# Kernel optimization log

Hardware: AMD Instinct MI355X
Metric: run time of the kernel (lower is better)

Reference implementation:

```python
import jax, jax.numpy as jnp
import numpy as np

SIG_T_TRAIN = 0.07
SIG_T_INFER = 0.07
EPS = 1e-12  # torch F.normalize eps


def _l2_normalize(x):
    # matches torch.nn.functional.normalize(x, dim=-1): x / max(||x||_2, eps)
    nrm = jnp.sqrt(jnp.sum(x * x, axis=-1, keepdims=True))
    return x / jnp.maximum(nrm, EPS)


def setup_inputs() -> dict:
    key = jax.random.key(0)
    k1, k2 = jax.random.split(key)
    v_feat = jax.random.normal(k1, (32, 16, 256, 512), dtype=jnp.float32)  # (b,n,t,d)
    t_feat = jax.random.normal(k2, (512, 512), dtype=jnp.float32)          # (c,d)
    return {"v_feat": v_feat, "t_feat": t_feat, "split": 1}


def reference(v_feat, t_feat, split):
    # split: 1 -> 'test' (normalize + sig_T_infer), 0 -> train (sig_T_train)
    if split == 1:
        tau = SIG_T_INFER
        v_feat = _l2_normalize(v_feat)
        t_feat = _l2_normalize(t_feat)
    else:
        tau = SIG_T_TRAIN
    # Original: dist = einsum('bntd,bmcd->bctnm', v, t_repeated)/tau, then mean over m, then n.
    # t_repeated is identical along m (a pure repeat), so mean over m is a no-op, and the
    # mean over n commutes with the linear contraction: reduce over n first, never
    # materializing the (b,c,t,n,m) tensor.
    v_mean = jnp.mean(v_feat, axis=1)  # (b,t,d)
    dist = jnp.einsum('btd,cd->bct', v_mean, t_feat) / tau  # (b,c,t)
    return dist
```

## Files before the change

### kernel.cpp

```cpp
#include <hip/hip_runtime.h>

typedef unsigned short u16;
typedef unsigned int u32;

typedef __bf16 bf16x8 __attribute__((ext_vector_type(8)));
typedef float f32x4 __attribute__((ext_vector_type(4)));

__device__ __forceinline__ u16 f2bf(float f) {
    u32 u = __float_as_uint(f);
    return (u16)((u + 0x7fffu + ((u >> 16) & 1u)) >> 16);
}

__device__ __forceinline__ float rowreduce64(float s) {
#pragma unroll
    for (int off = 32; off > 0; off >>= 1) s += __shfl_xor(s, off, 64);
    return s;
}

constexpr int LDK = 520;

__global__ __launch_bounds__(512, 2) void fused_kernel(
    const float* __restrict__ v,
    const float* __restrict__ tf,
    float* __restrict__ out,
    const int* __restrict__ splitp)
{
    const int b    = blockIdx.y;
    const int t0   = blockIdx.x * 32;
    const int tid  = threadIdx.x;
    const int w    = tid >> 6;
    const int lane = tid & 63;
    const int quad = lane >> 4;
    const int l15  = lane & 15;
    const int split = *splitp;

    __shared__ u16 At[64 * LDK];
    __shared__ u16 Bt[32 * LDK];

    for (int tt = 0; tt < 4; tt++) {
        const int tl = w * 4 + tt;
        float acc[8];
#pragma unroll
        for (int i = 0; i < 8; i++) acc[i] = 0.f;
#pragma unroll 4
        for (int n = 0; n < 16; n++) {
            const float* row = v + (((size_t)(b * 16 + n) * 256 + (t0 + tl)) * 512) + lane * 8;
            float4 x0 = *reinterpret_cast<const float4*>(row);
            float4 x1 = *reinterpret_cast<const float4*>(row + 4);
            float s = x0.x*x0.x + x0.y*x0.y + x0.z*x0.z + x0.w*x0.w
                    + x1.x*x1.x + x1.y*x1.y + x1.z*x1.z + x1.w*x1.w;
            s = rowreduce64(s);
            float inv = 1.0f;
            if (split == 1) inv = 1.0f / fmaxf(sqrtf(s), 1e-12f);
            acc[0] += x0.x*inv; acc[1] += x0.y*inv;
            acc[2] += x0.z*inv; acc[3] += x0.w*inv;
            acc[4] += x1.x*inv; acc[5] += x1.y*inv;
            acc[6] += x1.z*inv; acc[7] += x1.w*inv;
        }
        uint4 pk;
        pk.x = (u32)f2bf(acc[0]*0.0625f) | ((u32)f2bf(acc[1]*0.0625f) << 16);
        pk.y = (u32)f2bf(acc[2]*0.0625f) | ((u32)f2bf(acc[3]*0.0625f) << 16);
        pk.z = (u32)f2bf(acc[4]*0.0625f) | ((u32)f2bf(acc[5]*0.0625f) << 16);
        pk.w = (u32)f2bf(acc[6]*0.0625f) | ((u32)f2bf(acc[7]*0.0625f) << 16);
        *reinterpret_cast<uint4*>(&Bt[tl * LDK + lane * 8]) = pk;
    }

    const int wm = w & 3;
    const int wn = w >> 2;
    const float sc = 1.0f / 0.07f;
    float* ob = out + (size_t)b * 131072;

    for (int cc = 0; cc < 8; cc++) {
#pragma unroll
        for (int rr = 0; rr < 8; rr++) {
            const int r = w * 8 + rr;
            const float* rp = tf + (size_t)(cc * 64 + r) * 512 + lane * 8;
            float4 x0 = *reinterpret_cast<const float4*>(rp);
            float4 x1 = *reinterpret_cast<const float4*>(rp + 4);
            float s = x0.x*x0.x + x0.y*x0.y + x0.z*x0.z + x0.w*x0.w
                    + x1.x*x1.x + x1.y*x1.y + x1.z*x1.z + x1.w*x1.w;
            s = rowreduce64(s);
            float inv = 1.0f;
            if (split == 1) inv = 1.0f / fmaxf(sqrtf(s), 1e-12f);
            uint4 pk;
            pk.x = (u32)f2bf(x0.x*inv) | ((u32)f2bf(x0.y*inv) << 16);
            pk.y = (u32)f2bf(x0.z*inv) | ((u32)f2bf(x0.w*inv) << 16);
            pk.z = (u32)f2bf(x1.x*inv) | ((u32)f2bf(x1.y*inv) << 16);
            pk.w = (u32)f2bf(x1.z*inv) | ((u32)f2bf(x1.w*inv) << 16);
            *reinterpret_cast<uint4*>(&At[r * LDK + lane * 8]) = pk;
        }
        __syncthreads();

        f32x4 acc = {0.f, 0.f, 0.f, 0.f};
#pragma unroll
        for (int kk = 0; kk < 512; kk += 32) {
            bf16x8 af = *reinterpret_cast<const bf16x8*>(
                &At[(wm * 16 + l15) * LDK + kk + quad * 8]);
            bf16x8 bf = *reinterpret_cast<const bf16x8*>(
                &Bt[(wn * 16 + l15) * LDK + kk + quad * 8]);
            acc = __builtin_amdgcn_mfma_f32_16x16x32_bf16(af, bf, acc, 0, 0, 0);
        }
        __syncthreads();

#pragma unroll
        for (int r = 0; r < 4; r++) {
            const int c = cc * 64 + wm * 16 + quad * 4 + r;
            ob[c * 256 + (t0 + wn * 16 + l15)] = acc[r] * sc;
        }
    }
}

extern "C" void kernel_launch(void* const* d_in, const int* in_sizes, int n_in,
                              void* d_out, int out_size, void* d_ws, size_t ws_size,
                              hipStream_t stream) {
    const float* v_feat = (const float*)d_in[0];
    const float* t_feat = (const float*)d_in[1];
    const int*   splitp = (const int*)d_in[2];
    float* out = (float*)d_out;

    (void)d_ws; (void)ws_size;

    fused_kernel<<<dim3(8, 32), dim3(512), 0, stream>>>(v_feat, t_feat, out, splitp);
}
```

Before: 426.6 us.

## Split fused kernel into parallel prep pass and separate MFMA GEMM kernel

```diff
diff --git a/kernel.cpp b/kernel.cpp
--- a/kernel.cpp
+++ b/kernel.cpp
@@ -11,103 +11,148 @@
     return (u16)((u + 0x7fffu + ((u >> 16) & 1u)) >> 16);
 }
 
-__device__ __forceinline__ float rowreduce64(float s) {
-#pragma unroll
-    for (int off = 32; off > 0; off >>= 1) s += __shfl_xor(s, off, 64);
-    return s;
-}
-
-constexpr int LDK = 520;
-
-__global__ __launch_bounds__(512, 2) void fused_kernel(
+__global__ __launch_bounds__(256, 4) void prep_kernel(
     const float* __restrict__ v,
     const float* __restrict__ tf,
-    float* __restrict__ out,
+    u16* __restrict__ vm,
+    u16* __restrict__ tn,
     const int* __restrict__ splitp)
 {
-    const int b    = blockIdx.y;
-    const int t0   = blockIdx.x * 32;
     const int tid  = threadIdx.x;
     const int w    = tid >> 6;
     const int lane = tid & 63;
+    const int g    = lane >> 4;
+    const int l15  = lane & 15;
+    const int split = *splitp;
+    const int bxx  = blockIdx.x;
+
+    if (bxx >= 8192) {
+        const int row = (bxx - 8192) * 16 + w * 4 + g;
+        const float* rp = tf + (size_t)row * 512;
+        float4 x[8];
+#pragma unroll
+        for (int i = 0; i < 8; i++)
+            x[i] = *reinterpret_cast<const float4*>(rp + i * 64 + l15 * 4);
+        float s = 0.f;
+#pragma unroll
+        for (int i = 0; i < 8; i++)
+            s += x[i].x*x[i].x + x[i].y*x[i].y + x[i].z*x[i].z + x[i].w*x[i].w;
+#pragma unroll
+        for (int off = 1; off < 16; off <<= 1) s += __shfl_xor(s, off, 64);
+        float inv = 1.0f;
+        if (split == 1) inv = 1.0f / fmaxf(sqrtf(s), 1e-12f);
+        u16* orow = tn + (size_t)row * 512;
+#pragma unroll
+        for (int i = 0; i < 8; i++) {
+            uint2 pk;
+            pk.x = (u32)f2bf(x[i].x*inv) | ((u32)f2bf(x[i].y*inv) << 16);
+            pk.y = (u32)f2bf(x[i].z*inv) | ((u32)f2bf(x[i].w*inv) << 16);
+            *reinterpret_cast<uint2*>(orow + i * 64 + l15 * 4) = pk;
+        }
+        return;
+    }
+
+    const int b = bxx >> 8;
+    const int t = bxx & 255;
+    const int n = w * 4 + g;
+    const float* rp = v + (((size_t)(b * 16 + n) * 256) + t) * 512;
+
+    float4 x[8];
+#pragma unroll
+    for (int i = 0; i < 8; i++)
+        x[i] = *reinterpret_cast<const float4*>(rp + i * 64 + l15 * 4);
+
+    float s = 0.f;
+#pragma unroll
+    for (int i = 0; i < 8; i++)
+        s += x[i].x*x[i].x + x[i].y*x[i].y + x[i].z*x[i].z + x[i].w*x[i].w;
+#pragma unroll
+    for (int off = 1; off < 16; off <<= 1) s += __shfl_xor(s, off, 64);
+    float inv = 1.0f;
+    if (split == 1) inv = 1.0f / fmaxf(sqrtf(s), 1e-12f);
+
+#pragma unroll
+    for (int i = 0; i < 8; i++) {
+        x[i].x *= inv; x[i].y *= inv; x[i].z *= inv; x[i].w *= inv;
+    }
+
+#pragma unroll
+    for (int off = 16; off < 64; off <<= 1)
+#pragma unroll
+        for (int i = 0; i < 8; i++) {
+            x[i].x += __shfl_xor(x[i].x, off, 64);
+            x[i].y += __shfl_xor(x[i].y, off, 64);
+            x[i].z += __shfl_xor(x[i].z, off, 64);
+            x[i].w += __shfl_xor(x[i].w, off, 64);
+        }
+
+    __shared__ float lds[4][512];
+#pragma unroll
+    for (int j = 0; j < 2; j++) {
+        const int i = 2 * g + j;
+        *reinterpret_cast<float4*>(&lds[w][i * 64 + l15 * 4]) = x[i];
+    }
+    __syncthreads();
+
+    float2 r; r.x = 0.f; r.y = 0.f;
+#pragma unroll
+    for (int w2 = 0; w2 < 4; w2++) {
+        float2 p = *reinterpret_cast<const float2*>(&lds[w2][tid * 2]);
+        r.x += p.x; r.y += p.y;
+    }
+    r.x *= 0.0625f; r.y *= 0.0625f;
+    u32 packed = (u32)f2bf(r.x) | ((u32)f2bf(r.y) << 16);
+    reinterpret_cast<u32*>(vm)[((size_t)(b * 256 + t) << 8) + tid] = packed;
+}
+
+__global__ __launch_bounds__(256) void gemm_kernel(
+    const u16* __restrict__ tn,
+    const u16* __restrict__ vm,
+    float* __restrict__ out)
+{
+    const int tid  = threadIdx.x;
+    const int lane = tid & 63;
+    const int wid  = tid >> 6;
+    const int wm   = wid & 1;
+    const int wn   = wid >> 1;
     const int quad = lane >> 4;
     const int l15  = lane & 15;
-    const int split = *splitp;
 
-    __shared__ u16 At[64 * LDK];
-    __shared__ u16 Bt[32 * LDK];
+    const int c0 = blockIdx.x * 64 + wm * 32;
+    const int t0 = blockIdx.y * 64 + wn * 32;
+    const int b  = blockIdx.z;
 
-    for (int tt = 0; tt < 4; tt++) {
-        const int tl = w * 4 + tt;
-        float acc[8];
+    const u16* A0 = tn + (size_t)(c0 + l15) * 512 + quad * 8;
+    const u16* B0 = vm + (size_t)b * 131072 + (size_t)(t0 + l15) * 512 + quad * 8;
+
+    f32x4 acc[2][2] = {};
+#pragma unroll 4
+    for (int kk = 0; kk < 512; kk += 32) {
+        bf16x8 af[2], bf[2];
 #pragma unroll
-        for (int i = 0; i < 8; i++) acc[i] = 0.f;
-#pragma unroll 4
-        for (int n = 0; n < 16; n++) {
-            const float* row = v + (((size_t)(b * 16 + n) * 256 + (t0 + tl)) * 512) + lane * 8;
-            float4 x0 = *reinterpret_cast<const float4*>(row);
-            float4 x1 = *reinterpret_cast<const float4*>(row + 4);
-            float s = x0.x*x0.x + x0.y*x0.y + x0.z*x0.z + x0.w*x0.w
-                    + x1.x*x1.x + x1.y*x1.y + x1.z*x1.z + x1.w*x1.w;
-            s = rowreduce64(s);
-            float inv = 1.0f;
-            if (split == 1) inv = 1.0f / fmaxf(sqrtf(s), 1e-12f);
-            acc[0] += x0.x*inv; acc[1] += x0.y*inv;
-            acc[2] += x0.z*inv; acc[3] += x0.w*inv;
-            acc[4] += x1.x*inv; acc[5] += x1.y*inv;
-            acc[6] += x1.z*inv; acc[7] += x1.w*inv;
-        }
-        uint4 pk;
-        pk.x = (u32)f2bf(acc[0]*0.0625f) | ((u32)f2bf(acc[1]*0.0625f) << 16);
-        pk.y = (u32)f2bf(acc[2]*0.0625f) | ((u32)f2bf(acc[3]*0.0625f) << 16);
-        pk.z = (u32)f2bf(acc[4]*0.0625f) | ((u32)f2bf(acc[5]*0.0625f) << 16);
-        pk.w = (u32)f2bf(acc[6]*0.0625f) | ((u32)f2bf(acc[7]*0.0625f) << 16);
-        *reinterpret_cast<uint4*>(&Bt[tl * LDK + lane * 8]) = pk;
+        for (int i = 0; i < 2; i++)
+            af[i] = *reinterpret_cast<const bf16x8*>(A0 + (size_t)i * 16 * 512 + kk);
+#pragma unroll
+        for (int j = 0; j < 2; j++)
+            bf[j] = *reinterpret_cast<const bf16x8*>(B0 + (size_t)j * 16 * 512 + kk);
+#pragma unroll
+        for (int i = 0; i < 2; i++)
+#pragma unroll
+            for (int j = 0; j < 2; j++)
+                acc[i][j] = __builtin_amdgcn_mfma_f32_16x16x32_bf16(
+                    af[i], bf[j], acc[i][j], 0, 0, 0);
     }
 
-    const int wm = w & 3;
-    const int wn = w >> 2;
     const float sc = 1.0f / 0.07f;
     float* ob = out + (size_t)b * 131072;
-
-    for (int cc = 0; cc < 8; cc++) {
 #pragma unroll
-        for (int rr = 0; rr < 8; rr++) {
-            const int r = w * 8 + rr;
-            const float* rp = tf + (size_t)(cc * 64 + r) * 512 + lane * 8;
-            float4 x0 = *reinterpret_cast<const float4*>(rp);
-            float4 x1 = *reinterpret_cast<const float4*>(rp + 4);
-            float s = x0.x*x0.x + x0.y*x0.y + x0.z*x0.z + x0.w*x0.w
-                    + x1.x*x1.x + x1.y*x1.y + x1.z*x1.z + x1.w*x1.w;
-            s = rowreduce64(s);
-            float inv = 1.0f;
-            if (split == 1) inv = 1.0f / fmaxf(sqrtf(s), 1e-12f);
-            uint4 pk;
-            pk.x = (u32)f2bf(x0.x*inv) | ((u32)f2bf(x0.y*inv) << 16);
-            pk.y = (u32)f2bf(x0.z*inv) | ((u32)f2bf(x0.w*inv) << 16);
-            pk.z = (u32)f2bf(x1.x*inv) | ((u32)f2bf(x1.y*inv) << 16);
-            pk.w = (u32)f2bf(x1.z*inv) | ((u32)f2bf(x1.w*inv) << 16);
-            *reinterpret_cast<uint4*>(&At[r * LDK + lane * 8]) = pk;
-        }
-        __syncthreads();
-
-        f32x4 acc = {0.f, 0.f, 0.f, 0.f};
+    for (int i = 0; i < 2; i++)
 #pragma unroll
-        for (int kk = 0; kk < 512; kk += 32) {
-            bf16x8 af = *reinterpret_cast<const bf16x8*>(
-                &At[(wm * 16 + l15) * LDK + kk + quad * 8]);
-            bf16x8 bf = *reinterpret_cast<const bf16x8*>(
-                &Bt[(wn * 16 + l15) * LDK + kk + quad * 8]);
-            acc = __builtin_amdgcn_mfma_f32_16x16x32_bf16(af, bf, acc, 0, 0, 0);
-        }
-        __syncthreads();
-
+        for (int j = 0; j < 2; j++)
 #pragma unroll
-        for (int r = 0; r < 4; r++) {
-            const int c = cc * 64 + wm * 16 + quad * 4 + r;
-            ob[c * 256 + (t0 + wn * 16 + l15)] = acc[r] * sc;
-        }
-    }
+            for (int r = 0; r < 4; r++)
+                ob[(c0 + i * 16 + quad * 4 + r) * 256 + (t0 + j * 16 + l15)]
+                    = acc[i][j][r] * sc;
 }
 
 extern "C" void kernel_launch(void* const* d_in, const int* in_sizes, int n_in,
@@ -118,7 +163,9 @@
     const int*   splitp = (const int*)d_in[2];
     float* out = (float*)d_out;
 
-    (void)d_ws; (void)ws_size;
+    u16* tn = (u16*)d_ws;
+    u16* vm = tn + 512 * 512;
 
-    fused_kernel<<<dim3(8, 32), dim3(512), 0, stream>>>(v_feat, t_feat, out, splitp);
+    prep_kernel<<<dim3(8192 + 32), dim3(256), 0, stream>>>(v_feat, t_feat, vm, tn, splitp);
+    gemm_kernel<<<dim3(8, 4, 32), dim3(256), 0, stream>>>(tn, vm, out);
 }
```

Result: slower. 522.8 us (+22.5%).
